# Performance work log

Hardware: AMD Instinct MI355X
Metric: run time of the kernel (lower is better)

## Reference

```python
import jax, jax.numpy as jnp
import numpy as np

B, S, H, L = 64, 512, 1024, 9


def setup_inputs() -> dict:
    key = jax.random.key(0)
    k1, k2, k3, k4 = jax.random.split(key, 4)
    sequence_output = jax.random.normal(k1, (B, S, H), dtype=jnp.float32)
    valid_mask = jax.random.randint(k2, (B, S), 0, 2, dtype=jnp.int32)
    # classifier params (Dense(num_labels), TruncatedNormal(stddev=0.02) ~ normal here)
    W = jax.random.normal(k3, (H, L), dtype=jnp.float32) * 0.02
    b = jnp.zeros((L,), dtype=jnp.float32)
    return {"sequence_output": sequence_output, "valid_mask": valid_mask, "W": W, "b": b}


def _compact_valid(sequence_output, valid_mask):
    # Stable-sort tokens so valid (mask==1) tokens come first in original order,
    # then zero-pad the tail -- vectorized equivalent of the per-token Python loop.
    Bq, Sq, _ = sequence_output.shape
    pos = jnp.arange(Sq, dtype=jnp.int32)[None, :]                 # [1,S]
    sort_key = (1 - valid_mask) * Sq + pos                         # invalid pushed back, stable
    order = jnp.argsort(sort_key, axis=1)                          # [B,S]
    gathered = jnp.take_along_axis(sequence_output, order[:, :, None], axis=1)
    n_valid = jnp.sum(valid_mask, axis=1, keepdims=True)           # [B,1]
    keep = (pos < n_valid)[:, :, None]                             # [B,S,1]
    return jnp.where(keep, gathered, jnp.zeros((), sequence_output.dtype))


def reference(sequence_output, valid_mask, W, b):
    valid_output = _compact_valid(sequence_output, valid_mask)     # [B,S,H]
    # dropout is identity at inference (training=False)
    logits = jnp.einsum("bsh,hl->bsl", valid_output, W) + b
    return jax.nn.softmax(logits, axis=-1)
```

## Files before the change

### kernel.cpp

```cpp
#include <hip/hip_runtime.h>
#include <hip/hip_bf16.h>

#define BB 64
#define SS 512
#define HH 1024
#define LL 9

template <int CTRL>
__device__ __forceinline__ float dpp_add(float v) {
    int s = __builtin_bit_cast(int, v);
    int r = __builtin_amdgcn_update_dpp(0, s, CTRL, 0xF, 0xF, true);
    return v + __builtin_bit_cast(float, r);
}

__global__ __launch_bounds__(256) void fused_ner_kernel(
    const float* __restrict__ x, const int* __restrict__ mask,
    const float* __restrict__ W, const float* __restrict__ bias,
    float* __restrict__ out) {
    __shared__ __align__(16) float Wl[HH * LL];
    __shared__ int gidx_sh[SS];
    __shared__ int wsum[4];
    __shared__ float bsh[LL];
    __shared__ float obuf[64 * LL];

    const int tid  = threadIdx.x;
    const int bat  = blockIdx.x & 63;
    const int blk  = blockIdx.x >> 6;
    const int lane = tid & 63;
    const int wv_  = tid >> 6;

    #pragma unroll
    for (int i = 0; i < 9; ++i) {
        const int f4 = i * 256 + tid;
        __builtin_amdgcn_global_load_lds(
            (const __attribute__((address_space(1))) void*)(W + f4 * 4),
            (__attribute__((address_space(3))) void*)(&Wl[f4 * 4]),
            16, 0, 0);
    }
    if (tid < LL) bsh[tid] = bias[tid];

    const int2 mm = reinterpret_cast<const int2*>(mask + bat * SS)[tid];
    const int m0 = mm.x, m1 = mm.y;
    const int s = m0 + m1;
    int incl = s;
    #pragma unroll
    for (int off = 1; off < 64; off <<= 1) {
        int u = __shfl_up(incl, off, 64);
        if (lane >= off) incl += u;
    }
    if (lane == 63) wsum[wv_] = incl;
    __syncthreads();
    int wbase = 0;
    #pragma unroll
    for (int i = 0; i < 4; ++i) if (i < wv_) wbase += wsum[i];
    const int nv = wsum[0] + wsum[1] + wsum[2] + wsum[3];
    const int excl = incl - s + wbase;
    if (m0) gidx_sh[excl] = 2 * tid;
    if (m1) gidx_sh[excl + m0] = 2 * tid + 1;
    __syncthreads();

    const int jbeg = (blk * nv) >> 3;
    const int jend = ((blk + 1) * nv) >> 3;
    const int nwork = jend - jbeg;
    const int npad = SS - nv;
    const int pbeg = nv + ((blk * npad) >> 3);
    const int pend = nv + (((blk + 1) * npad) >> 3);

    const int g = lane >> 4;
    const int k = lane & 15;

    #pragma unroll 1
    for (int pass = 0; pass < 4; ++pass) {
        const int lp0 = pass * 16 + wv_ * 4;
        if (lp0 >= nwork) break;

        float sc[4];
        const float4* xr[4];
        #pragma unroll
        for (int r = 0; r < 4; ++r) {
            const int j = jbeg + lp0 + r;
            const bool valid = (j < jend);
            sc[r] = valid ? 1.f : 0.f;
            const int src = gidx_sh[valid ? j : jbeg];
            xr[r] = reinterpret_cast<const float4*>(x + ((size_t)bat * SS + src) * HH);
        }

        float4 xq[4][4];
        #pragma unroll
        for (int i = 0; i < 4; ++i)
            #pragma unroll
            for (int r = 0; r < 4; ++r) xq[r][i] = xr[r][i * 64 + lane];

        float acc[4][LL];
        #pragma unroll
        for (int r = 0; r < 4; ++r)
            #pragma unroll
            for (int l = 0; l < LL; ++l) acc[r][l] = 0.f;

        #pragma unroll
        for (int i = 0; i < 4; ++i) {
            float4 wb[9];
            const float* wp = &Wl[(i * 64 + lane) * 36];
            #pragma unroll
            for (int j2 = 0; j2 < 9; ++j2)
                wb[j2] = *reinterpret_cast<const float4*>(wp + j2 * 4);
            const float* wf = reinterpret_cast<const float*>(wb);

            #pragma unroll
            for (int l = 0; l < LL; ++l) {
                #pragma unroll
                for (int r = 0; r < 4; ++r) {
                    const float4 xvv = xq[r][i];
                    acc[r][l] += xvv.x * wf[0 * 9 + l] + xvv.y * wf[1 * 9 + l]
                               + xvv.z * wf[2 * 9 + l] + xvv.w * wf[3 * 9 + l];
                }
            }
        }

        #pragma unroll
        for (int r = 0; r < 4; ++r)
            #pragma unroll
            for (int l = 0; l < LL; ++l) {
                float v = acc[r][l];
                v = dpp_add<0x111>(v);
                v = dpp_add<0x112>(v);
                v = dpp_add<0x114>(v);
                v = dpp_add<0x118>(v);
                v += __shfl_xor(v, 16, 64);
                v += __shfl_xor(v, 32, 64);
                acc[r][l] = v;
            }

        float lg[LL];
        #pragma unroll
        for (int l = 0; l < LL; ++l) {
            float v = acc[0][l] * sc[0];
            if (g == 1) v = acc[1][l] * sc[1];
            if (g == 2) v = acc[2][l] * sc[2];
            if (g == 3) v = acc[3][l] * sc[3];
            lg[l] = v + bsh[l];
        }
        float mx = -3.0e38f;
        #pragma unroll
        for (int l = 0; l < LL; ++l) mx = fmaxf(mx, lg[l]);
        float ssum = 0.f;
        #pragma unroll
        for (int l = 0; l < LL; ++l) { lg[l] = __expf(lg[l] - mx); ssum += lg[l]; }
        const float inv = 1.f / ssum;
        if (k == 15) {
            #pragma unroll
            for (int l = 0; l < LL; ++l) obuf[(lp0 + g) * LL + l] = lg[l] * inv;
        }
    }

    float bs[LL];
    float mxb = -3.0e38f;
    #pragma unroll
    for (int l = 0; l < LL; ++l) { bs[l] = bsh[l]; mxb = fmaxf(mxb, bs[l]); }
    float sb = 0.f;
    #pragma unroll
    for (int l = 0; l < LL; ++l) { bs[l] = __expf(bs[l] - mxb); sb += bs[l]; }
    const float invb = 1.f / sb;

    __syncthreads();

    const size_t vbase = ((size_t)bat * SS + jbeg) * LL;
    for (int t = tid; t < nwork * LL; t += 256) out[vbase + t] = obuf[t];

    const size_t pbase = ((size_t)bat * SS + pbeg) * LL;
    const int pn = (pend - pbeg) * LL;
    for (int t = tid; t < pn; t += 256) {
        const int row = t / LL;
        const int l   = t - row * LL;
        out[pbase + t] = bs[l] * invb;
    }
}

extern "C" void kernel_launch(void* const* d_in, const int* in_sizes, int n_in,
                              void* d_out, int out_size, void* d_ws, size_t ws_size,
                              hipStream_t stream) {
    const float* x    = (const float*)d_in[0];
    const int*   mask = (const int*)d_in[1];
    const float* W    = (const float*)d_in[2];
    const float* bias = (const float*)d_in[3];
    float* out = (float*)d_out;

    fused_ner_kernel<<<BB * 8, 256, 0, stream>>>(x, mask, W, bias, out);
}
```

Baseline: 24.14 us.

## Hoist W slice into registers, halve rows per pass, use DPP row-broadcast reduction

Each lane now loads its 144 W coefficients from LDS into registers once, before the row loop, instead of re-reading them every pass. To make room in the register budget, each wave handles 2 rows per pass instead of 4, with twice as many passes. The cross-row shuffles are replaced by DPP row_bcast15/31 steps, and softmax runs only on lane 63. Launch bounds request 2 blocks per SM. The risk is register pressure and spills from holding 144 weight floats, plus less memory-level parallelism with fewer rows in flight per pass.

```diff
diff --git a/kernel.cpp b/kernel.cpp
--- a/kernel.cpp
+++ b/kernel.cpp
@@ -13,7 +13,7 @@
     return v + __builtin_bit_cast(float, r);
 }
 
-__global__ __launch_bounds__(256) void fused_ner_kernel(
+__global__ __launch_bounds__(256, 2) void fused_ner_kernel(
     const float* __restrict__ x, const int* __restrict__ mask,
     const float* __restrict__ W, const float* __restrict__ bias,
     float* __restrict__ out) {
@@ -59,6 +59,20 @@
     if (m1) gidx_sh[excl + m0] = 2 * tid + 1;
     __syncthreads();
 
+    float wf[4][36];
+    #pragma unroll
+    for (int i = 0; i < 4; ++i) {
+        const float* wp = &Wl[(i * 64 + lane) * 36];
+        #pragma unroll
+        for (int j = 0; j < 9; ++j) {
+            const float4 t = *reinterpret_cast<const float4*>(wp + j * 4);
+            wf[i][j * 4 + 0] = t.x;
+            wf[i][j * 4 + 1] = t.y;
+            wf[i][j * 4 + 2] = t.z;
+            wf[i][j * 4 + 3] = t.w;
+        }
+    }
+
     const int jbeg = (blk * nv) >> 3;
     const int jend = ((blk + 1) * nv) >> 3;
     const int nwork = jend - jbeg;
@@ -66,18 +80,15 @@
     const int pbeg = nv + ((blk * npad) >> 3);
     const int pend = nv + (((blk + 1) * npad) >> 3);
 
-    const int g = lane >> 4;
-    const int k = lane & 15;
-
     #pragma unroll 1
-    for (int pass = 0; pass < 4; ++pass) {
-        const int lp0 = pass * 16 + wv_ * 4;
+    for (int pass = 0; pass < 8; ++pass) {
+        const int lp0 = pass * 8 + wv_ * 2;
         if (lp0 >= nwork) break;
 
-        float sc[4];
-        const float4* xr[4];
+        float sc[2];
+        const float4* xr[2];
         #pragma unroll
-        for (int r = 0; r < 4; ++r) {
+        for (int r = 0; r < 2; ++r) {
             const int j = jbeg + lp0 + r;
             const bool valid = (j < jend);
             sc[r] = valid ? 1.f : 0.f;
@@ -85,40 +96,33 @@
             xr[r] = reinterpret_cast<const float4*>(x + ((size_t)bat * SS + src) * HH);
         }
 
-        float4 xq[4][4];
+        float4 xq[2][4];
         #pragma unroll
         for (int i = 0; i < 4; ++i)
             #pragma unroll
-            for (int r = 0; r < 4; ++r) xq[r][i] = xr[r][i * 64 + lane];
+            for (int r = 0; r < 2; ++r) xq[r][i] = xr[r][i * 64 + lane];
 
-        float acc[4][LL];
+        float acc[2][LL];
         #pragma unroll
-        for (int r = 0; r < 4; ++r)
+        for (int r = 0; r < 2; ++r)
             #pragma unroll
             for (int l = 0; l < LL; ++l) acc[r][l] = 0.f;
 
         #pragma unroll
         for (int i = 0; i < 4; ++i) {
-            float4 wb[9];
-            const float* wp = &Wl[(i * 64 + lane) * 36];
-            #pragma unroll
-            for (int j2 = 0; j2 < 9; ++j2)
-                wb[j2] = *reinterpret_cast<const float4*>(wp + j2 * 4);
-            const float* wf = reinterpret_cast<const float*>(wb);
-
             #pragma unroll
             for (int l = 0; l < LL; ++l) {
                 #pragma unroll
-                for (int r = 0; r < 4; ++r) {
+                for (int r = 0; r < 2; ++r) {
                     const float4 xvv = xq[r][i];
-                    acc[r][l] += xvv.x * wf[0 * 9 + l] + xvv.y * wf[1 * 9 + l]
-                               + xvv.z * wf[2 * 9 + l] + xvv.w * wf[3 * 9 + l];
+                    acc[r][l] += xvv.x * wf[i][0 * 9 + l] + xvv.y * wf[i][1 * 9 + l]
+                               + xvv.z * wf[i][2 * 9 + l] + xvv.w * wf[i][3 * 9 + l];
                 }
             }
         }
 
         #pragma unroll
-        for (int r = 0; r < 4; ++r)
+        for (int r = 0; r < 2; ++r)
             #pragma unroll
             for (int l = 0; l < LL; ++l) {
                 float v = acc[r][l];
@@ -126,30 +130,28 @@
                 v = dpp_add<0x112>(v);
                 v = dpp_add<0x114>(v);
                 v = dpp_add<0x118>(v);
-                v += __shfl_xor(v, 16, 64);
-                v += __shfl_xor(v, 32, 64);
+                v = dpp_add<0x142>(v);
+                v = dpp_add<0x143>(v);
                 acc[r][l] = v;
             }
 
-        float lg[LL];
-        #pragma unroll
-        for (int l = 0; l < LL; ++l) {
-            float v = acc[0][l] * sc[0];
-            if (g == 1) v = acc[1][l] * sc[1];
-            if (g == 2) v = acc[2][l] * sc[2];
-            if (g == 3) v = acc[3][l] * sc[3];
-            lg[l] = v + bsh[l];
-        }
-        float mx = -3.0e38f;
-        #pragma unroll
-        for (int l = 0; l < LL; ++l) mx = fmaxf(mx, lg[l]);
-        float ssum = 0.f;
-        #pragma unroll
-        for (int l = 0; l < LL; ++l) { lg[l] = __expf(lg[l] - mx); ssum += lg[l]; }
-        const float inv = 1.f / ssum;
-        if (k == 15) {
+        if (lane == 63) {
             #pragma unroll
-            for (int l = 0; l < LL; ++l) obuf[(lp0 + g) * LL + l] = lg[l] * inv;
+            for (int r = 0; r < 2; ++r) {
+                float lg[LL];
+                float mx = -3.0e38f;
+                #pragma unroll
+                for (int l = 0; l < LL; ++l) {
+                    lg[l] = acc[r][l] * sc[r] + bsh[l];
+                    mx = fmaxf(mx, lg[l]);
+                }
+                float ssum = 0.f;
+                #pragma unroll
+                for (int l = 0; l < LL; ++l) { lg[l] = __expf(lg[l] - mx); ssum += lg[l]; }
+                const float inv = 1.f / ssum;
+                #pragma unroll
+                for (int l = 0; l < LL; ++l) obuf[(lp0 + r) * LL + l] = lg[l] * inv;
+            }
         }
     }
 
```

New measurement: 22.76 us. 1.06x faster.
